# Kernel optimization log

Measured on AMD Instinct MI355X. Metric: run time of the kernel, lower is better.

Reference implementation:

```python
import jax, jax.numpy as jnp
import numpy as np

N_NODES = 16
N_EDGES = 64
N_LAYERS = 4


def _gcn(x, src, dst, emask, W, b):
    # PyG GCNConv: add self-loops, symmetric deg^-1/2 normalization, sum-aggregate.
    n = x.shape[0]
    h = x @ W  # [n, d_out]
    deg = jax.ops.segment_sum(emask, dst, num_segments=n) + 1.0  # +1 self-loop
    dinv = jax.lax.rsqrt(deg)
    norm = dinv[src] * dinv[dst] * emask  # masked-out edges get 0 weight
    out = jax.ops.segment_sum(norm[:, None] * h[src], dst, num_segments=n)
    return out + (dinv * dinv)[:, None] * h + b  # self-loop term + bias


def _sag_pool(x, src, dst, emask, w_rel, b_rel, w_root, k):
    # SAGPooling with GraphConv scorer: score = lin_rel(sum_j x_j) + lin_root(x)
    n = x.shape[0]
    agg = jax.ops.segment_sum(emask[:, None] * x[src], dst, num_segments=n)
    score = agg @ w_rel + b_rel + x @ w_root  # [n]
    perm = jnp.argsort(-score)[:k]  # top-k nodes
    x_new = x[perm] * jnp.tanh(score[perm])[:, None]
    kept = jnp.zeros(n, bool).at[perm].set(True)
    pos = jnp.zeros(n, jnp.int32).at[perm].set(jnp.arange(k, dtype=jnp.int32))
    emask_new = emask * kept[src] * kept[dst]  # drop edges touching removed nodes
    return x_new, pos[src], pos[dst], emask_new


def _conv_gnn(x, src, dst, W0, Ws, bs, pWrel, pbrel, pWroot, linW, linb):
    emask = jnp.ones(src.shape[0], x.dtype)
    n = x.shape[0]
    for i in range(N_LAYERS):
        W = W0 if i == 0 else Ws[i - 1]
        x = jax.nn.relu(_gcn(x, src, dst, emask, W, bs[i]))
        k = -(-n // 2)  # ceil(0.5 * n) -- SAGPooling ratio=0.5
        x, src, dst, emask = _sag_pool(x, src, dst, emask, pWrel[i], pbrel[i], pWroot[i], k)
        n = k
    x = x @ linW + linb  # [1, 128]
    return jax.nn.log_softmax(x, axis=1)


def _fc(h, fcW, fcb, lnw, lnb):
    eps = 1e-5
    for i in range(3):
        h = h @ fcW[i] + fcb[i]
        mu = h.mean(-1, keepdims=True)
        var = ((h - mu) ** 2).mean(-1, keepdims=True)
        h = (h - mu) * jax.lax.rsqrt(var + eps) * lnw[i] + lnb[i]
        h = jax.nn.relu(h)
    return h @ fcW[3] + fcb[3]


def setup_inputs() -> dict:
    key = jax.random.key(0)
    ks = iter(jax.random.split(key, 64))

    def rn(shape, s=0.05):
        return jax.random.normal(next(ks), shape, jnp.float32) * s

    def gnn_params(p):
        return {
            p + '_W0': rn((45, 128)), p + '_W': rn((3, 128, 128)),
            p + '_b': jnp.zeros((4, 128), jnp.float32),
            p + '_pWrel': rn((4, 128)), p + '_pbrel': jnp.zeros((4,), jnp.float32),
            p + '_pWroot': rn((4, 128)),
            p + '_linW': rn((128, 128)), p + '_linb': jnp.zeros((128,), jnp.float32),
        }

    inp = {
        'gp_x': rn((N_NODES, 45), 1.0), 'sp_x': rn((N_NODES, 45), 1.0),
        'gp_src': jax.random.randint(next(ks), (N_EDGES,), 0, N_NODES, jnp.int32),
        'gp_dst': jax.random.randint(next(ks), (N_EDGES,), 0, N_NODES, jnp.int32),
        'sp_src': jax.random.randint(next(ks), (N_EDGES,), 0, N_NODES, jnp.int32),
        'sp_dst': jax.random.randint(next(ks), (N_EDGES,), 0, N_NODES, jnp.int32),
        'fcW': rn((4, 256, 256)), 'fcb': jnp.zeros((4, 256), jnp.float32),
        'lnw': jnp.ones((3, 256), jnp.float32), 'lnb': jnp.zeros((3, 256), jnp.float32),
    }
    inp.update(gnn_params('g'))
    inp.update(gnn_params('s'))
    return inp


def reference(gp_x, sp_x, gp_src, gp_dst, sp_src, sp_dst,
              g_W0, g_W, g_b, g_pWrel, g_pbrel, g_pWroot, g_linW, g_linb,
              s_W0, s_W, s_b, s_pWrel, s_pbrel, s_pWroot, s_linW, s_linb,
              fcW, fcb, lnw, lnb):
    out1 = _conv_gnn(gp_x, gp_src, gp_dst, g_W0, g_W, g_b, g_pWrel, g_pbrel, g_pWroot, g_linW, g_linb)
    out2 = _conv_gnn(sp_x, sp_src, sp_dst, s_W0, s_W, s_b, s_pWrel, s_pbrel, s_pWroot, s_linW, s_linb)
    concat = jnp.concatenate((out1.reshape(-1), out2.reshape(-1)))  # [256]
    return _fc(concat, fcW, fcb, lnw, lnb)
```

## Files before the change

kernel.cpp:

```cpp
#include <hip/hip_runtime.h>
#include <math.h>

#define MAGIC 0x5F3759DFu
typedef unsigned int u32;

__device__ __forceinline__ void bar_lds(){
  asm volatile("s_waitcnt lgkmcnt(0)\n\ts_barrier" ::: "memory");
}
__device__ __forceinline__ void bar_vm0(){
  asm volatile("s_waitcnt vmcnt(0) lgkmcnt(0)\n\ts_barrier" ::: "memory");
}
__device__ __forceinline__ void bar_vm8(){
  asm volatile("s_waitcnt vmcnt(8) lgkmcnt(0)\n\ts_barrier" ::: "memory");
}

__device__ inline float wsum(float v){
  #pragma unroll
  for (int o=32;o;o>>=1) v += __shfl_xor(v,o,64);
  return v;
}
__device__ inline float wmax(float v){
  #pragma unroll
  for (int o=32;o;o>>=1) v = fmaxf(v,__shfl_xor(v,o,64));
  return v;
}
__device__ inline float hsum32(float v){
  #pragma unroll
  for (int o=16;o;o>>=1) v += __shfl_xor(v,o,64);
  return v;
}
__device__ __forceinline__ void stageW(const float* g, float* l, int nfloats,
                                       int wid, int lane){
  const int nch = nfloats>>8;
  for (int c=wid; c<nch; c+=8)
    __builtin_amdgcn_global_load_lds(
      (__attribute__((address_space(1))) u32*)(void*)(g+(c<<8)+(lane<<2)),
      (__attribute__((address_space(3))) u32*)(void*)(l+(c<<8)), 16, 0, 0);
}
__device__ __forceinline__ void pf(const float* p, int nfloats, int tid){
  float4 acc={0.f,0.f,0.f,0.f};
  const int nq=nfloats>>2;
  for (int i=tid;i<nq;i+=512){
    const float4 v=((const float4*)p)[i];
    acc.x+=v.x; acc.y+=v.y; acc.z+=v.z; acc.w+=v.w;
  }
  asm volatile("" :: "v"(acc.x),"v"(acc.y),"v"(acc.z),"v"(acc.w));
}

__global__ __launch_bounds__(512,1) void net_kernel(
    const float* __restrict__ gp_x, const float* __restrict__ sp_x,
    const int* __restrict__ gp_src, const int* __restrict__ gp_dst,
    const int* __restrict__ sp_src, const int* __restrict__ sp_dst,
    const float* __restrict__ g_W0, const float* __restrict__ g_W,
    const float* __restrict__ g_b,  const float* __restrict__ g_pWrel,
    const float* __restrict__ g_pbrel, const float* __restrict__ g_pWroot,
    const float* __restrict__ g_linW, const float* __restrict__ g_linb,
    const float* __restrict__ s_W0, const float* __restrict__ s_W,
    const float* __restrict__ s_b,  const float* __restrict__ s_pWrel,
    const float* __restrict__ s_pbrel, const float* __restrict__ s_pWroot,
    const float* __restrict__ s_linW, const float* __restrict__ s_linb,
    const float* __restrict__ fcW, const float* __restrict__ fcb,
    const float* __restrict__ lnw, const float* __restrict__ lnb,
    float* __restrict__ wsbuf, float* __restrict__ out)
{
  __shared__ __align__(16) float slotA[16384];
  __shared__ __align__(16) float slotB[16384];
  __shared__ __align__(16) float XBx[16][128];
  __shared__ __align__(16) float ZBraw[1024];
  __shared__ __align__(16) float PBf[2048];
  __shared__ __align__(16) float wrelL[512], wrootL[512];
  __shared__ __align__(16) float Adn[256], Mdn[256];
  __shared__ float d1P[64], d2P[64];
  __shared__ float yA[128];
  __shared__ float tsA[8]; __shared__ int permA[8];
  __shared__ float fcin[256]; __shared__ float wpart[16];

  const int lt  = threadIdx.x;
  const int bid = blockIdx.x;
  const int wid = lt>>6, lane = lt&63;

  if (bid >= 6){
    if (bid==6){ pf(g_W0,5760,lt); pf(g_pWrel,512,lt); pf(g_pWroot,512,lt);
                 pf(g_b,512,lt);   pf(g_linb,128,lt); }
    else if (bid==7){ pf(s_W0,5760,lt); pf(s_pWrel,512,lt); pf(s_pWroot,512,lt);
                 pf(s_b,512,lt);   pf(s_linb,128,lt); }
    else if (bid<=11) pf(g_W + (bid-8)*12288, 12288, lt);
    else if (bid<=15) pf(s_W + (bid-12)*12288, 12288, lt);
    else if (bid<=17) pf(g_linW + (bid-16)*8192, 8192, lt);
    else              pf(s_linW + (bid-18)*8192, 8192, lt);
    return;
  }

  if (bid >= 2){
    const int L = bid-2;
    const int qfc=(wid<<3)+(lane&7), f0fc=(lane>>3)<<5;
    float4 wr[32];
    #pragma unroll
    for (int t=0;t<32;++t) wr[t]=*(const float4*)(fcW+(L<<16)+(f0fc+t)*256+(qfc<<2));
    const float4 bb=*(const float4*)(fcb+(L<<8)+(qfc<<2));
    float4 lw={0,0,0,0}, lb2={0,0,0,0};
    if (L<3){ lw=*(const float4*)(lnw+(L<<8)+(qfc<<2)); lb2=*(const float4*)(lnb+(L<<8)+(qfc<<2)); }
    if (lt==0){
      if (L==0){
        const u32* f1=(const u32*)(wsbuf+128);
        const u32* f2=(const u32*)(wsbuf+384);
        while (__hip_atomic_load(f1,__ATOMIC_ACQUIRE,__HIP_MEMORY_SCOPE_AGENT)!=MAGIC ||
               __hip_atomic_load(f2,__ATOMIC_ACQUIRE,__HIP_MEMORY_SCOPE_AGENT)!=MAGIC)
          __builtin_amdgcn_s_sleep(1);
      } else {
        const u32* f1=(const u32*)(wsbuf+512+(L-1)*512+256);
        while (__hip_atomic_load(f1,__ATOMIC_ACQUIRE,__HIP_MEMORY_SCOPE_AGENT)!=MAGIC)
          __builtin_amdgcn_s_sleep(1);
      }
    }
    bar_lds();
    if (lt<256){
      const float* src = (L==0) ? (wsbuf + (lt<128 ? lt : 128+lt))
                                : (wsbuf + 512 + (L-1)*512 + lt);
      fcin[lt]=__hip_atomic_load(src,__ATOMIC_RELAXED,__HIP_MEMORY_SCOPE_AGENT);
    }
    bar_lds();
    float4 a={0.f,0.f,0.f,0.f};
    #pragma unroll
    for (int t=0;t<32;++t){
      const float zv=fcin[f0fc+t];
      a.x+=zv*wr[t].x; a.y+=zv*wr[t].y; a.z+=zv*wr[t].z; a.w+=zv*wr[t].w;
    }
    #pragma unroll
    for (int m=8;m<64;m<<=1){
      a.x+=__shfl_xor(a.x,m,64); a.y+=__shfl_xor(a.y,m,64);
      a.z+=__shfl_xor(a.z,m,64); a.w+=__shfl_xor(a.w,m,64);
    }
    if (L==3){
      if (lane<8){
        float4 r; r.x=a.x+bb.x; r.y=a.y+bb.y; r.z=a.z+bb.z; r.w=a.w+bb.w;
        *(float4*)(out+(qfc<<2))=r;
      }
      return;
    }
    const bool act=(lane<8);
    float4 hv={0.f,0.f,0.f,0.f};
    if (act){
      hv.x=a.x+bb.x; hv.y=a.y+bb.y; hv.z=a.z+bb.z; hv.w=a.w+bb.w;
      float s=hv.x+hv.y+hv.z+hv.w;
      float s2=hv.x*hv.x+hv.y*hv.y+hv.z*hv.z+hv.w*hv.w;
      #pragma unroll
      for (int m=1;m<8;m<<=1){ s+=__shfl_xor(s,m,64); s2+=__shfl_xor(s2,m,64); }
      if (lane==0){ wpart[wid]=s; wpart[8+wid]=s2; }
    }
    bar_lds();
    if (act){
      float S=0.f,S2=0.f;
      #pragma unroll
      for (int w2=0;w2<8;++w2){ S+=wpart[w2]; S2+=wpart[8+w2]; }
      const float mu=S*(1.f/256.f);
      const float ri=rsqrtf(S2*(1.f/256.f)-mu*mu+1e-5f);
      float* dst=wsbuf+512+L*512+(qfc<<2);
      __hip_atomic_store(dst+0,fmaxf((hv.x-mu)*ri*lw.x+lb2.x,0.f),__ATOMIC_RELAXED,__HIP_MEMORY_SCOPE_AGENT);
      __hip_atomic_store(dst+1,fmaxf((hv.y-mu)*ri*lw.y+lb2.y,0.f),__ATOMIC_RELAXED,__HIP_MEMORY_SCOPE_AGENT);
      __hip_atomic_store(dst+2,fmaxf((hv.z-mu)*ri*lw.z+lb2.z,0.f),__ATOMIC_RELAXED,__HIP_MEMORY_SCOPE_AGENT);
      __hip_atomic_store(dst+3,fmaxf((hv.w-mu)*ri*lw.w+lb2.w,0.f),__ATOMIC_RELAXED,__HIP_MEMORY_SCOPE_AGENT);
    }
    __threadfence();
    bar_lds();
    if (lt==0) __hip_atomic_store((u32*)(wsbuf+512+L*512+256),MAGIC,__ATOMIC_RELEASE,__HIP_MEMORY_SCOPE_AGENT);
    return;
  }

  const int br = bid;
  const float* x0    = br ? sp_x    : gp_x;
  const int*   srcg  = br ? sp_src  : gp_src;
  const int*   dstg  = br ? sp_dst  : gp_dst;
  const float* W0    = br ? s_W0    : g_W0;
  const float* Wl    = br ? s_W     : g_W;
  const float* bl    = br ? s_b     : g_b;
  const float* wrel  = br ? s_pWrel : g_pWrel;
  const float* brel  = br ? s_pbrel : g_pbrel;
  const float* wroot = br ? s_pWroot: g_pWroot;
  const float* linWg = br ? s_linW  : g_linW;
  const float* linb  = br ? s_linb  : g_linb;
  float* wsOut = wsbuf + br*256;
  u32*   wsFlag = (u32*)(wsbuf + 128 + br*256);

  float xv[4];
  #pragma unroll
  for (int r=0;r<4;++r){
    const int i=lt+(r<<9), v=i>>7, f=i&127;
    xv[r] = (f<45)? x0[v*45+f] : 0.f;
  }
  int es=0, ed=0; float emk=0.f;
  if (lt<64){ es=srcg[lt]; ed=dstg[lt]; emk=1.f; }
  const float4 brelv = *(const float4*)brel;
  const int bi4=(lt&31)<<2;
  const float4 blv0=*(const float4*)(bl       + bi4);
  const float4 blv1=*(const float4*)(bl + 128 + bi4);
  const float4 blv2=*(const float4*)(bl + 256 + bi4);
  const float4 blv3=*(const float4*)(bl + 384 + bi4);
  const float linb_s = linb[lt>>2];
  asm volatile("" ::: "memory");
  stageW(wrel,  wrelL,  512, wid, lane);
  stageW(wroot, wrootL, 512, wid, lane);
  stageW(Wl,    slotA, 16384, wid, lane);

  auto build_dense=[&](int kk, float wlane, bool with_ts){
    const float4 z4={0.f,0.f,0.f,0.f};
    *(float4*)&Adn[lt<<2]=z4;
    *(float4*)&Mdn[lt<<2]=z4;
    const bool act=(emk!=0.f);
    int mycnt=0;
    for (int v=0;v<kk;++v){
      const unsigned long long m=__ballot(act&&(ed==v));
      if (lt==v) mycnt=__popcll(m);
    }
    const float dinvl=rsqrtf(1.f+(float)mycnt);
    const float dvs=__shfl(dinvl,es,64);
    const float dvd=__shfl(dinvl,ed,64);
    if (act){
      atomicAdd(&Adn[ed*16+es], dvs*dvd*wlane);
      atomicAdd(&Mdn[ed*16+es], 1.f);
    }
    if (lt<kk){
      const float tv = with_ts ? tsA[lt] : 1.f;
      atomicAdd(&Adn[lt*17], dinvl*dinvl*tv);
    }
  };
  auto doE=[&](int n,int k,float bv,bool rebuild){
    if (lt<64){
      const float d1s=(lt<n)? d1P[lt<<2] : 0.f;
      float sc=-INFINITY;
      if (lt<n){
        float acc=d2P[lt<<2]+bv;
        for (int u=0;u<n;++u) acc += Mdn[lt*16+u]*__shfl(d1s,u,64);
        sc=acc;
      }
      int rank=0;
      for (int u=0;u<n;++u){
        const float su=__shfl(sc,u,64);
        rank += (su>sc || (su==sc && u<lt)) ? 1:0;
      }
      const int kept=(lt<n && rank<k)?1:0;
      const int pos=kept?rank:0;
      const float tval=kept?tanhf(sc):0.f;
      if (kept){ permA[rank]=lt; tsA[rank]=tval; }
      const float ts_src=__shfl(tval,es,64);
      const int ks=__shfl(kept,es,64), kd=__shfl(kept,ed,64);
      const int ps=__shfl(pos,es,64),  pd=__shfl(pos,ed,64);
      emk *= (float)(ks&kd);
      es=ps; ed=pd;
      if (rebuild) build_dense(k, ts_src, true);
    }
  };
  auto doB=[&](int n){
    if (lt<(n<<5)){
      const int v=lt>>5, j4=(lt&31)<<2;
      float4 a={0.f,0.f,0.f,0.f};
      for (int u=0;u<n;++u){
        const float w=Adn[v*16+u];
        const float4 xs=*(const float4*)&XBx[permA[u]][j4];
        a.x+=w*xs.x; a.y+=w*xs.y; a.z+=w*xs.z; a.w+=w*xs.w;
      }
      *(float4*)&ZBraw[(v<<7)+j4]=a;
    }
  };
  auto cmain=[&](const float* slot, int L){
    const int sh=9-L, nq=512>>L, CH=128>>L;
    const int q=lt&(nq-1), fh=lt>>sh;
    const int v=q>>5, c4=q&31, f0=fh*CH;
    const float* zrow=&ZBraw[v<<7];
    float4 a={0.f,0.f,0.f,0.f};
    for (int f=0; f<CH; ++f){
      const float zv=zrow[f0+f];
      const float4 w4=*(const float4*)&slot[(f0+f)*128+(c4<<2)];
      a.x+=zv*w4.x; a.y+=zv*w4.y; a.z+=zv*w4.z; a.w+=zv*w4.w;
    }
    ((float4*)PBf)[lt]=a;
  };
  auto creduce=[&](int L, float4 bl4){
    const int nq=512>>L, SPL=1<<L;
    if (lt<nq){
      const int v=lt>>5, c4=lt&31;
      float4 acc=bl4;
      for (int s=0;s<SPL;++s){
        const float4 p=((const float4*)PBf)[s*nq+lt];
        acc.x+=p.x; acc.y+=p.y; acc.z+=p.z; acc.w+=p.w;
      }
      float4 o;
      o.x=fmaxf(acc.x,0.f); o.y=fmaxf(acc.y,0.f);
      o.z=fmaxf(acc.z,0.f); o.w=fmaxf(acc.w,0.f);
      *(float4*)&XBx[v][c4<<2]=o;
      const float4 wr4=*(const float4*)&wrelL[(L<<7)+(c4<<2)];
      const float4 wo4=*(const float4*)&wrootL[(L<<7)+(c4<<2)];
      float p1=o.x*wr4.x+o.y*wr4.y+o.z*wr4.z+o.w*wr4.w;
      float p2=o.x*wo4.x+o.y*wo4.y+o.z*wo4.z+o.w*wo4.w;
      p1=hsum32(p1); p2=hsum32(p2);
      if ((lane&31)==0){ d1P[v<<2]=p1; d2P[v<<2]=p2; }
    }
  };

  #pragma unroll
  for (int r=0;r<4;++r){
    const int i=lt+(r<<9), v=i>>7, f=i&127;
    XBx[v][f]=xv[r];
  }
  if (lt<64) build_dense(16, 1.f, false);
  bar_lds();

  if (lt<256){
    const int v=lt>>4, j4=(lt&15)<<2;
    if (j4<48){
      float4 a={0.f,0.f,0.f,0.f};
      for (int u=0;u<16;++u){
        const float w=Adn[v*16+u];
        const float4 xs=*(const float4*)&XBx[u][j4];
        a.x+=w*xs.x; a.y+=w*xs.y; a.z+=w*xs.z; a.w+=w*xs.w;
      }
      *(float4*)&ZBraw[v*48+j4]=a;
    }
  }
  bar_vm8();

  {
    const int v=lt>>5, c4=lt&31, j4=c4<<2;
    const float* zrow=&ZBraw[v*48];
    float4 a={0.f,0.f,0.f,0.f};
    #pragma unroll
    for (int bb=0;bb<2;++bb){
      float4 wr[16]; float zr[16];
      #pragma unroll
      for (int t=0;t<16;++t){ wr[t]=*(const float4*)(W0+(bb*16+t)*128+j4); zr[t]=zrow[bb*16+t]; }
      #pragma unroll
      for (int t=0;t<16;++t){ a.x+=zr[t]*wr[t].x; a.y+=zr[t]*wr[t].y; a.z+=zr[t]*wr[t].z; a.w+=zr[t]*wr[t].w; }
    }
    { float4 wr[13]; float zr[13];
      #pragma unroll
      for (int t=0;t<13;++t){ wr[t]=*(const float4*)(W0+(32+t)*128+j4); zr[t]=zrow[32+t]; }
      #pragma unroll
      for (int t=0;t<13;++t){ a.x+=zr[t]*wr[t].x; a.y+=zr[t]*wr[t].y; a.z+=zr[t]*wr[t].z; a.w+=zr[t]*wr[t].w; }
    }
    float4 ox;
    ox.x=fmaxf(a.x+blv0.x,0.f); ox.y=fmaxf(a.y+blv0.y,0.f);
    ox.z=fmaxf(a.z+blv0.z,0.f); ox.w=fmaxf(a.w+blv0.w,0.f);
    *(float4*)&XBx[v][j4]=ox;
    const float4 wr4=*(const float4*)&wrelL[j4];
    const float4 wo4=*(const float4*)&wrootL[j4];
    float p1=ox.x*wr4.x+ox.y*wr4.y+ox.z*wr4.z+ox.w*wr4.w;
    float p2=ox.x*wo4.x+ox.y*wo4.y+ox.z*wo4.z+ox.w*wo4.w;
    p1=hsum32(p1); p2=hsum32(p2);
    if ((lane&31)==0){
      const int vv=(wid<<1)|(lane>>5);
      d1P[vv<<2]=p1; d2P[vv<<2]=p2;
    }
  }
  stageW(Wl+16384, slotB, 16384, wid, lane);
  bar_lds();

  doE(16, 8, brelv.x, true);   bar_lds();
  doB(8);                      bar_vm8();
  cmain(slotA, 1);             bar_lds();
  creduce(1, blv1);            bar_lds();
  stageW(Wl+32768, slotA, 16384, wid, lane);
  doE(8, 4, brelv.y, true);    bar_lds();
  doB(4);                      bar_vm8();
  cmain(slotB, 2);             bar_lds();
  creduce(2, blv2);            bar_lds();
  stageW(linWg, slotB, 16384, wid, lane);
  doE(4, 2, brelv.z, true);    bar_lds();
  doB(2);                      bar_vm8();
  cmain(slotA, 3);             bar_lds();
  creduce(3, blv3);            bar_lds();
  doE(2, 1, brelv.w, false);   bar_vm0();

  {
    const int oj=lt>>2, fh=lt&3;
    const int prow=permA[0];
    float p=0.f;
    #pragma unroll
    for (int i=0;i<32;++i){
      const int f=(fh<<5)+i;
      p += XBx[prow][f]*slotB[f*128+oj];
    }
    p+=__shfl_xor(p,1,64); p+=__shfl_xor(p,2,64);
    if (fh==0) yA[oj]=p*tsA[0]+linb_s;
  }
  bar_lds();
  if (lt<128){
    const int ln=lt&63;
    const float a0=yA[ln], b0=yA[64+ln];
    const float m=wmax(fmaxf(a0,b0));
    const float sum=wsum(expf(a0-m)+expf(b0-m));
    const float lse=m+logf(sum);
    __hip_atomic_store(&wsOut[lt], yA[lt]-lse, __ATOMIC_RELAXED, __HIP_MEMORY_SCOPE_AGENT);
  }
  __threadfence();
  bar_lds();
  if (lt==0) __hip_atomic_store(wsFlag, MAGIC, __ATOMIC_RELEASE, __HIP_MEMORY_SCOPE_AGENT);
}

extern "C" void kernel_launch(void* const* d_in, const int* in_sizes, int n_in,
                              void* d_out, int out_size, void* d_ws, size_t ws_size,
                              hipStream_t stream){
  net_kernel<<<20,512,0,stream>>>(
    (const float*)d_in[0],(const float*)d_in[1],
    (const int*)d_in[2],(const int*)d_in[3],(const int*)d_in[4],(const int*)d_in[5],
    (const float*)d_in[10],(const float*)d_in[11],(const float*)d_in[12],(const float*)d_in[13],
    (const float*)d_in[14],(const float*)d_in[15],(const float*)d_in[16],(const float*)d_in[17],
    (const float*)d_in[18],(const float*)d_in[19],(const float*)d_in[20],(const float*)d_in[21],
    (const float*)d_in[22],(const float*)d_in[23],(const float*)d_in[24],(const float*)d_in[25],
    (const float*)d_in[6],(const float*)d_in[7],(const float*)d_in[8],(const float*)d_in[9],
    (float*)d_ws,(float*)d_out);
}
```

Measured before the change: 24.18 us.

## Fold first FC layer partials into GNN branch blocks to shorten the chain

Result: slower. 25.16 us (+4.0%).

```diff
diff --git a/kernel.cpp b/kernel.cpp
--- a/kernel.cpp
+++ b/kernel.cpp
@@ -45,6 +45,20 @@
     acc.x+=v.x; acc.y+=v.y; acc.z+=v.z; acc.w+=v.w;
   }
   asm volatile("" :: "v"(acc.x),"v"(acc.y),"v"(acc.z),"v"(acc.w));
+}
+__device__ __forceinline__ void poll1(const u32* f, int lane){
+  u32 v=0;
+  do {
+    if (lane==0) v=__hip_atomic_load(f,__ATOMIC_ACQUIRE,__HIP_MEMORY_SCOPE_AGENT);
+    v=(u32)__shfl((int)v,0,64);
+    if (v!=MAGIC) __builtin_amdgcn_s_sleep(1);
+  } while (v!=MAGIC);
+}
+__device__ __forceinline__ float aload(const float* p){
+  return __hip_atomic_load(p,__ATOMIC_RELAXED,__HIP_MEMORY_SCOPE_AGENT);
+}
+__device__ __forceinline__ void astore(float* p, float v){
+  __hip_atomic_store(p,v,__ATOMIC_RELAXED,__HIP_MEMORY_SCOPE_AGENT);
 }
 
 __global__ __launch_bounds__(512,1) void net_kernel(
@@ -78,60 +92,107 @@
   const int lt  = threadIdx.x;
   const int bid = blockIdx.x;
   const int wid = lt>>6, lane = lt&63;
-
-  if (bid >= 6){
-    if (bid==6){ pf(g_W0,5760,lt); pf(g_pWrel,512,lt); pf(g_pWroot,512,lt);
+  const int qfc=(wid<<3)+(lane&7);
+
+  if (bid >= 5){
+    if (bid==5){ pf(g_W0,5760,lt); pf(g_pWrel,512,lt); pf(g_pWroot,512,lt);
                  pf(g_b,512,lt);   pf(g_linb,128,lt); }
-    else if (bid==7){ pf(s_W0,5760,lt); pf(s_pWrel,512,lt); pf(s_pWroot,512,lt);
+    else if (bid==6){ pf(s_W0,5760,lt); pf(s_pWrel,512,lt); pf(s_pWroot,512,lt);
                  pf(s_b,512,lt);   pf(s_linb,128,lt); }
-    else if (bid<=11) pf(g_W + (bid-8)*12288, 12288, lt);
-    else if (bid<=15) pf(s_W + (bid-12)*12288, 12288, lt);
-    else if (bid<=17) pf(g_linW + (bid-16)*8192, 8192, lt);
-    else              pf(s_linW + (bid-18)*8192, 8192, lt);
+    else if (bid<=10) pf(g_W + (bid-7)*12288, 12288, lt);
+    else if (bid<=14) pf(s_W + (bid-11)*12288, 12288, lt);
+    else if (bid<=16) pf(g_linW + (bid-15)*8192, 8192, lt);
+    else if (bid<=18) pf(s_linW + (bid-17)*8192, 8192, lt);
+    else if (bid==19) pf(fcW, 32768, lt);
+    else              pf(fcW+32768, 32768, lt);
     return;
   }
 
   if (bid >= 2){
-    const int L = bid-2;
-    const int qfc=(wid<<3)+(lane&7), f0fc=(lane>>3)<<5;
+    const int L = bid-1;
+    const int f0fc=(lane>>3)<<5;
     float4 wr[32];
     #pragma unroll
     for (int t=0;t<32;++t) wr[t]=*(const float4*)(fcW+(L<<16)+(f0fc+t)*256+(qfc<<2));
     const float4 bb=*(const float4*)(fcb+(L<<8)+(qfc<<2));
     float4 lw={0,0,0,0}, lb2={0,0,0,0};
     if (L<3){ lw=*(const float4*)(lnw+(L<<8)+(qfc<<2)); lb2=*(const float4*)(lnb+(L<<8)+(qfc<<2)); }
-    if (lt==0){
-      if (L==0){
-        const u32* f1=(const u32*)(wsbuf+128);
-        const u32* f2=(const u32*)(wsbuf+384);
-        while (__hip_atomic_load(f1,__ATOMIC_ACQUIRE,__HIP_MEMORY_SCOPE_AGENT)!=MAGIC ||
-               __hip_atomic_load(f2,__ATOMIC_ACQUIRE,__HIP_MEMORY_SCOPE_AGENT)!=MAGIC)
-          __builtin_amdgcn_s_sleep(1);
-      } else {
-        const u32* f1=(const u32*)(wsbuf+512+(L-1)*512+256);
-        while (__hip_atomic_load(f1,__ATOMIC_ACQUIRE,__HIP_MEMORY_SCOPE_AGENT)!=MAGIC)
-          __builtin_amdgcn_s_sleep(1);
-      }
-    }
-    bar_lds();
-    if (lt<256){
-      const float* src = (L==0) ? (wsbuf + (lt<128 ? lt : 128+lt))
-                                : (wsbuf + 512 + (L-1)*512 + lt);
-      fcin[lt]=__hip_atomic_load(src,__ATOMIC_RELAXED,__HIP_MEMORY_SCOPE_AGENT);
-    }
-    bar_lds();
+
+    if (bid==2){
+      float b0=0.f,w0=0.f,l0=0.f;
+      if (lt<256){ b0=fcb[lt]; w0=lnw[lt]; l0=lnb[lt]; }
+      poll1((const u32*)(wsbuf+256), lane);
+      poll1((const u32*)(wsbuf+576), lane);
+      float h=0.f;
+      if (lt<256){
+        h = aload(wsbuf+lt) + aload(wsbuf+320+lt) + b0;
+        float s=wsum(h), s2=wsum(h*h);
+        if (lane==0){ wpart[wid]=s; wpart[8+wid]=s2; }
+      }
+      bar_lds();
+      if (lt<256){
+        const float S =wpart[0]+wpart[1]+wpart[2]+wpart[3];
+        const float S2=wpart[8]+wpart[9]+wpart[10]+wpart[11];
+        const float mu=S*(1.f/256.f);
+        const float ri=rsqrtf(S2*(1.f/256.f)-mu*mu+1e-5f);
+        fcin[lt]=fmaxf((h-mu)*ri*w0+l0,0.f);
+      }
+      bar_lds();
+      float4 a={0.f,0.f,0.f,0.f};
+      #pragma unroll
+      for (int t=0;t<32;++t){
+        const float zv=fcin[f0fc+t];
+        a.x+=zv*wr[t].x; a.y+=zv*wr[t].y; a.z+=zv*wr[t].z; a.w+=zv*wr[t].w;
+      }
+      #pragma unroll
+      for (int m=8;m<64;m<<=1){
+        a.x+=__shfl_xor(a.x,m,64); a.y+=__shfl_xor(a.y,m,64);
+        a.z+=__shfl_xor(a.z,m,64); a.w+=__shfl_xor(a.w,m,64);
+      }
+      const bool act=(lane<8);
+      float4 hv={0.f,0.f,0.f,0.f};
+      if (act){
+        hv.x=a.x+bb.x; hv.y=a.y+bb.y; hv.z=a.z+bb.z; hv.w=a.w+bb.w;
+        float s=hv.x+hv.y+hv.z+hv.w;
+        float s2=hv.x*hv.x+hv.y*hv.y+hv.z*hv.z+hv.w*hv.w;
+        #pragma unroll
+        for (int m=1;m<8;m<<=1){ s+=__shfl_xor(s,m,64); s2+=__shfl_xor(s2,m,64); }
+        if (lane==0){ wpart[wid]=s; wpart[8+wid]=s2; }
+      }
+      bar_lds();
+      if (act){
+        float S=0.f,S2=0.f;
+        #pragma unroll
+        for (int w2=0;w2<8;++w2){ S+=wpart[w2]; S2+=wpart[8+w2]; }
+        const float mu=S*(1.f/256.f);
+        const float ri=rsqrtf(S2*(1.f/256.f)-mu*mu+1e-5f);
+        float* dst=wsbuf+640+(qfc<<2);
+        astore(dst+0,fmaxf((hv.x-mu)*ri*lw.x+lb2.x,0.f));
+        astore(dst+1,fmaxf((hv.y-mu)*ri*lw.y+lb2.y,0.f));
+        astore(dst+2,fmaxf((hv.z-mu)*ri*lw.z+lb2.z,0.f));
+        astore(dst+3,fmaxf((hv.w-mu)*ri*lw.w+lb2.w,0.f));
+      }
+      bar_vm0();
+      if (lt==0) __hip_atomic_store((u32*)(wsbuf+896),MAGIC,__ATOMIC_RELEASE,__HIP_MEMORY_SCOPE_AGENT);
+      return;
+    }
+
+    const int srcoff=(bid==3)?640:960, floff=(bid==3)?896:1216;
+    poll1((const u32*)(wsbuf+floff), lane);
+    float zr[32];
+    #pragma unroll
+    for (int t=0;t<32;++t) zr[t]=aload(wsbuf+srcoff+f0fc+t);
     float4 a={0.f,0.f,0.f,0.f};
     #pragma unroll
     for (int t=0;t<32;++t){
-      const float zv=fcin[f0fc+t];
-      a.x+=zv*wr[t].x; a.y+=zv*wr[t].y; a.z+=zv*wr[t].z; a.w+=zv*wr[t].w;
+      a.x+=zr[t]*wr[t].x; a.y+=zr[t]*wr[t].y; a.z+=zr[t]*wr[t].z; a.w+=zr[t]*wr[t].w;
     }
     #pragma unroll
     for (int m=8;m<64;m<<=1){
       a.x+=__shfl_xor(a.x,m,64); a.y+=__shfl_xor(a.y,m,64);
       a.z+=__shfl_xor(a.z,m,64); a.w+=__shfl_xor(a.w,m,64);
     }
-    if (L==3){
+    if (bid==4){
       if (lane<8){
         float4 r; r.x=a.x+bb.x; r.y=a.y+bb.y; r.z=a.z+bb.z; r.w=a.w+bb.w;
         *(float4*)(out+(qfc<<2))=r;
@@ -155,15 +216,14 @@
       for (int w2=0;w2<8;++w2){ S+=wpart[w2]; S2+=wpart[8+w2]; }
       const float mu=S*(1.f/256.f);
       const float ri=rsqrtf(S2*(1.f/256.f)-mu*mu+1e-5f);
-      float* dst=wsbuf+512+L*512+(qfc<<2);
-      __hip_atomic_store(dst+0,fmaxf((hv.x-mu)*ri*lw.x+lb2.x,0.f),__ATOMIC_RELAXED,__HIP_MEMORY_SCOPE_AGENT);
-      __hip_atomic_store(dst+1,fmaxf((hv.y-mu)*ri*lw.y+lb2.y,0.f),__ATOMIC_RELAXED,__HIP_MEMORY_SCOPE_AGENT);
-      __hip_atomic_store(dst+2,fmaxf((hv.z-mu)*ri*lw.z+lb2.z,0.f),__ATOMIC_RELAXED,__HIP_MEMORY_SCOPE_AGENT);
-      __hip_atomic_store(dst+3,fmaxf((hv.w-mu)*ri*lw.w+lb2.w,0.f),__ATOMIC_RELAXED,__HIP_MEMORY_SCOPE_AGENT);
-    }
-    __threadfence();
-    bar_lds();
-    if (lt==0) __hip_atomic_store((u32*)(wsbuf+512+L*512+256),MAGIC,__ATOMIC_RELEASE,__HIP_MEMORY_SCOPE_AGENT);
+      float* dst=wsbuf+960+(qfc<<2);
+      astore(dst+0,fmaxf((hv.x-mu)*ri*lw.x+lb2.x,0.f));
+      astore(dst+1,fmaxf((hv.y-mu)*ri*lw.y+lb2.y,0.f));
+      astore(dst+2,fmaxf((hv.z-mu)*ri*lw.z+lb2.z,0.f));
+      astore(dst+3,fmaxf((hv.w-mu)*ri*lw.w+lb2.w,0.f));
+    }
+    bar_vm0();
+    if (lt==0) __hip_atomic_store((u32*)(wsbuf+1216),MAGIC,__ATOMIC_RELEASE,__HIP_MEMORY_SCOPE_AGENT);
     return;
   }
 
@@ -179,8 +239,9 @@
   const float* wroot = br ? s_pWroot: g_pWroot;
   const float* linWg = br ? s_linW  : g_linW;
   const float* linb  = br ? s_linb  : g_linb;
-  float* wsOut = wsbuf + br*256;
-  u32*   wsFlag = (u32*)(wsbuf + 128 + br*256);
+  float* wsOut = wsbuf + br*320;
+  u32*   wsFlag = (u32*)(wsbuf + 256 + br*320);
+  const int f0fc=(lane>>3)<<4;
 
   float xv[4];
   #pragma unroll
@@ -352,6 +413,10 @@
     }
   }
   stageW(Wl+16384, slotB, 16384, wid, lane);
+  float4 wfc[16];
+  #pragma unroll
+  for (int t=0;t<16;++t)
+    wfc[t]=*(const float4*)(fcW + ((br<<7)+f0fc+t)*256 + (qfc<<2));
   bar_lds();
 
   doE(16, 8, brelv.x, true);   bar_lds();
@@ -389,17 +454,34 @@
     const float m=wmax(fmaxf(a0,b0));
     const float sum=wsum(expf(a0-m)+expf(b0-m));
     const float lse=m+logf(sum);
-    __hip_atomic_store(&wsOut[lt], yA[lt]-lse, __ATOMIC_RELAXED, __HIP_MEMORY_SCOPE_AGENT);
-  }
-  __threadfence();
+    fcin[lt]=yA[lt]-lse;
+  }
   bar_lds();
+  {
+    float4 a={0.f,0.f,0.f,0.f};
+    #pragma unroll
+    for (int t=0;t<16;++t){
+      const float zv=fcin[f0fc+t];
+      a.x+=zv*wfc[t].x; a.y+=zv*wfc[t].y; a.z+=zv*wfc[t].z; a.w+=zv*wfc[t].w;
+    }
+    #pragma unroll
+    for (int m=8;m<64;m<<=1){
+      a.x+=__shfl_xor(a.x,m,64); a.y+=__shfl_xor(a.y,m,64);
+      a.z+=__shfl_xor(a.z,m,64); a.w+=__shfl_xor(a.w,m,64);
+    }
+    if (lane<8){
+      float* dst=wsOut+(qfc<<2);
+      astore(dst+0,a.x); astore(dst+1,a.y); astore(dst+2,a.z); astore(dst+3,a.w);
+    }
+  }
+  bar_vm0();
   if (lt==0) __hip_atomic_store(wsFlag, MAGIC, __ATOMIC_RELEASE, __HIP_MEMORY_SCOPE_AGENT);
 }
 
 extern "C" void kernel_launch(void* const* d_in, const int* in_sizes, int n_in,
                               void* d_out, int out_size, void* d_ws, size_t ws_size,
                               hipStream_t stream){
-  net_kernel<<<20,512,0,stream>>>(
+  net_kernel<<<21,512,0,stream>>>(
     (const float*)d_in[0],(const float*)d_in[1],
     (const int*)d_in[2],(const int*)d_in[3],(const int*)d_in[4],(const int*)d_in[5],
     (const float*)d_in[10],(const float*)d_in[11],(const float*)d_in[12],(const float*)d_in[13],
```

## Poll flags per wave, load FC inputs directly, retile GCN matmul partials

Applied to the files above, without the earlier changes.

After: 24.17 us. About the same (-0.1%).

```diff
diff --git a/kernel.cpp b/kernel.cpp
--- a/kernel.cpp
+++ b/kernel.cpp
@@ -45,6 +45,56 @@
     acc.x+=v.x; acc.y+=v.y; acc.z+=v.z; acc.w+=v.w;
   }
   asm volatile("" :: "v"(acc.x),"v"(acc.y),"v"(acc.z),"v"(acc.w));
+}
+__device__ __forceinline__ void poll1(const u32* f, int lane){
+  u32 v=0;
+  do {
+    if (lane==0) v=__hip_atomic_load(f,__ATOMIC_ACQUIRE,__HIP_MEMORY_SCOPE_AGENT);
+    v=(u32)__shfl((int)v,0,64);
+    if (v!=MAGIC) __builtin_amdgcn_s_sleep(1);
+  } while (v!=MAGIC);
+}
+__device__ __forceinline__ float aload(const float* p){
+  return __hip_atomic_load(p,__ATOMIC_RELAXED,__HIP_MEMORY_SCOPE_AGENT);
+}
+__device__ __forceinline__ void astore(float* p, float v){
+  __hip_atomic_store(p,v,__ATOMIC_RELAXED,__HIP_MEMORY_SCOPE_AGENT);
+}
+
+template<int F,int VH,int N>
+__device__ __forceinline__ void cmain2(int lt, const float* slot,
+                                       const float* ZBp, float* PBp){
+  constexpr int CH = 128/F;
+  const int c4 = lt&31, r = lt>>5;
+  const int fh = r & (F-1), vh = r / F;
+  const int f0 = fh*CH;
+  const float4* slot4 = (const float4*)slot;
+  float4 acc[VH];
+  #pragma unroll
+  for (int i=0;i<VH;++i) acc[i]=make_float4(0.f,0.f,0.f,0.f);
+  #pragma unroll
+  for (int f=0; f<CH; ++f){
+    const float4 w4 = slot4[(f0+f)*32 + c4];
+    #pragma unroll
+    for (int i=0;i<VH;++i){
+      const float zv = ZBp[((vh*VH+i)<<7) + f0 + f];
+      acc[i].x+=zv*w4.x; acc[i].y+=zv*w4.y; acc[i].z+=zv*w4.z; acc[i].w+=zv*w4.w;
+    }
+  }
+  #pragma unroll
+  for (int i=0;i<VH;++i){
+    acc[i].x+=__shfl_xor(acc[i].x,32,64);
+    acc[i].y+=__shfl_xor(acc[i].y,32,64);
+    acc[i].z+=__shfl_xor(acc[i].z,32,64);
+    acc[i].w+=__shfl_xor(acc[i].w,32,64);
+  }
+  if (!(r&1)){
+    const int fp = fh>>1;
+    float4* P4=(float4*)PBp;
+    #pragma unroll
+    for (int i=0;i<VH;++i)
+      P4[(fp*N + vh*VH + i)*32 + c4] = acc[i];
+  }
 }
 
 __global__ __launch_bounds__(512,1) void net_kernel(
@@ -100,31 +150,29 @@
     const float4 bb=*(const float4*)(fcb+(L<<8)+(qfc<<2));
     float4 lw={0,0,0,0}, lb2={0,0,0,0};
     if (L<3){ lw=*(const float4*)(lnw+(L<<8)+(qfc<<2)); lb2=*(const float4*)(lnb+(L<<8)+(qfc<<2)); }
-    if (lt==0){
-      if (L==0){
-        const u32* f1=(const u32*)(wsbuf+128);
-        const u32* f2=(const u32*)(wsbuf+384);
-        while (__hip_atomic_load(f1,__ATOMIC_ACQUIRE,__HIP_MEMORY_SCOPE_AGENT)!=MAGIC ||
-               __hip_atomic_load(f2,__ATOMIC_ACQUIRE,__HIP_MEMORY_SCOPE_AGENT)!=MAGIC)
-          __builtin_amdgcn_s_sleep(1);
-      } else {
-        const u32* f1=(const u32*)(wsbuf+512+(L-1)*512+256);
-        while (__hip_atomic_load(f1,__ATOMIC_ACQUIRE,__HIP_MEMORY_SCOPE_AGENT)!=MAGIC)
-          __builtin_amdgcn_s_sleep(1);
-      }
-    }
-    bar_lds();
-    if (lt<256){
-      const float* src = (L==0) ? (wsbuf + (lt<128 ? lt : 128+lt))
-                                : (wsbuf + 512 + (L-1)*512 + lt);
-      fcin[lt]=__hip_atomic_load(src,__ATOMIC_RELAXED,__HIP_MEMORY_SCOPE_AGENT);
-    }
-    bar_lds();
+
+    float zr[32];
+    if (L==0){
+      poll1((const u32*)(wsbuf+128), lane);
+      poll1((const u32*)(wsbuf+384), lane);
+      if (lt<256){
+        const float* src = wsbuf + (lt<128 ? lt : 128+lt);
+        fcin[lt]=aload(src);
+      }
+      bar_lds();
+      #pragma unroll
+      for (int t=0;t<32;++t) zr[t]=fcin[f0fc+t];
+    } else {
+      const int floff = (L==1)?768 : (L==2)?1280 : 1792;
+      const int srcoff= (L==1)?512 : (L==2)?1024 : 1536;
+      poll1((const u32*)(wsbuf+floff), lane);
+      #pragma unroll
+      for (int t=0;t<32;++t) zr[t]=aload(wsbuf+srcoff+f0fc+t);
+    }
     float4 a={0.f,0.f,0.f,0.f};
     #pragma unroll
     for (int t=0;t<32;++t){
-      const float zv=fcin[f0fc+t];
-      a.x+=zv*wr[t].x; a.y+=zv*wr[t].y; a.z+=zv*wr[t].z; a.w+=zv*wr[t].w;
+      a.x+=zr[t]*wr[t].x; a.y+=zr[t]*wr[t].y; a.z+=zr[t]*wr[t].z; a.w+=zr[t]*wr[t].w;
     }
     #pragma unroll
     for (int m=8;m<64;m<<=1){
@@ -156,13 +204,12 @@
       const float mu=S*(1.f/256.f);
       const float ri=rsqrtf(S2*(1.f/256.f)-mu*mu+1e-5f);
       float* dst=wsbuf+512+L*512+(qfc<<2);
-      __hip_atomic_store(dst+0,fmaxf((hv.x-mu)*ri*lw.x+lb2.x,0.f),__ATOMIC_RELAXED,__HIP_MEMORY_SCOPE_AGENT);
-      __hip_atomic_store(dst+1,fmaxf((hv.y-mu)*ri*lw.y+lb2.y,0.f),__ATOMIC_RELAXED,__HIP_MEMORY_SCOPE_AGENT);
-      __hip_atomic_store(dst+2,fmaxf((hv.z-mu)*ri*lw.z+lb2.z,0.f),__ATOMIC_RELAXED,__HIP_MEMORY_SCOPE_AGENT);
-      __hip_atomic_store(dst+3,fmaxf((hv.w-mu)*ri*lw.w+lb2.w,0.f),__ATOMIC_RELAXED,__HIP_MEMORY_SCOPE_AGENT);
-    }
-    __threadfence();
-    bar_lds();
+      astore(dst+0,fmaxf((hv.x-mu)*ri*lw.x+lb2.x,0.f));
+      astore(dst+1,fmaxf((hv.y-mu)*ri*lw.y+lb2.y,0.f));
+      astore(dst+2,fmaxf((hv.z-mu)*ri*lw.z+lb2.z,0.f));
+      astore(dst+3,fmaxf((hv.w-mu)*ri*lw.w+lb2.w,0.f));
+    }
+    bar_vm0();
     if (lt==0) __hip_atomic_store((u32*)(wsbuf+512+L*512+256),MAGIC,__ATOMIC_RELEASE,__HIP_MEMORY_SCOPE_AGENT);
     return;
   }
@@ -262,26 +309,13 @@
       *(float4*)&ZBraw[(v<<7)+j4]=a;
     }
   };
-  auto cmain=[&](const float* slot, int L){
-    const int sh=9-L, nq=512>>L, CH=128>>L;
-    const int q=lt&(nq-1), fh=lt>>sh;
-    const int v=q>>5, c4=q&31, f0=fh*CH;
-    const float* zrow=&ZBraw[v<<7];
-    float4 a={0.f,0.f,0.f,0.f};
-    for (int f=0; f<CH; ++f){
-      const float zv=zrow[f0+f];
-      const float4 w4=*(const float4*)&slot[(f0+f)*128+(c4<<2)];
-      a.x+=zv*w4.x; a.y+=zv*w4.y; a.z+=zv*w4.z; a.w+=zv*w4.w;
-    }
-    ((float4*)PBf)[lt]=a;
-  };
-  auto creduce=[&](int L, float4 bl4){
-    const int nq=512>>L, SPL=1<<L;
-    if (lt<nq){
+  auto creduce2=[&](int F, int N, int L, float4 bl4){
+    if (lt < (N<<5)){
       const int v=lt>>5, c4=lt&31;
+      const float4* P4=(const float4*)PBf;
       float4 acc=bl4;
-      for (int s=0;s<SPL;++s){
-        const float4 p=((const float4*)PBf)[s*nq+lt];
+      for (int fp=0; fp<(F>>1); ++fp){
+        const float4 p=P4[(fp*N+v)*32+c4];
         acc.x+=p.x; acc.y+=p.y; acc.z+=p.z; acc.w+=p.w;
       }
       float4 o;
@@ -354,21 +388,21 @@
   stageW(Wl+16384, slotB, 16384, wid, lane);
   bar_lds();
 
-  doE(16, 8, brelv.x, true);   bar_lds();
-  doB(8);                      bar_vm8();
-  cmain(slotA, 1);             bar_lds();
-  creduce(1, blv1);            bar_lds();
+  doE(16, 8, brelv.x, true);    bar_lds();
+  doB(8);                       bar_vm8();
+  cmain2<4,2,8>(lt, slotA, ZBraw, PBf);  bar_lds();
+  creduce2(4, 8, 1, blv1);      bar_lds();
   stageW(Wl+32768, slotA, 16384, wid, lane);
-  doE(8, 4, brelv.y, true);    bar_lds();
-  doB(4);                      bar_vm8();
-  cmain(slotB, 2);             bar_lds();
-  creduce(2, blv2);            bar_lds();
+  doE(8, 4, brelv.y, true);     bar_lds();
+  doB(4);                       bar_vm8();
+  cmain2<8,2,4>(lt, slotB, ZBraw, PBf); bar_lds();
+  creduce2(8, 4, 2, blv2);      bar_lds();
   stageW(linWg, slotB, 16384, wid, lane);
-  doE(4, 2, brelv.z, true);    bar_lds();
-  doB(2);                      bar_vm8();
-  cmain(slotA, 3);             bar_lds();
-  creduce(3, blv3);            bar_lds();
-  doE(2, 1, brelv.w, false);   bar_vm0();
+  doE(4, 2, brelv.z, true);     bar_lds();
+  doB(2);                       bar_vm8();
+  cmain2<8,1,2>(lt, slotA, ZBraw, PBf); bar_lds();
+  creduce2(8, 2, 3, blv3);      bar_lds();
+  doE(2, 1, brelv.w, false);    bar_vm0();
 
   {
     const int oj=lt>>2, fh=lt&3;
@@ -389,10 +423,9 @@
     const float m=wmax(fmaxf(a0,b0));
     const float sum=wsum(expf(a0-m)+expf(b0-m));
     const float lse=m+logf(sum);
-    __hip_atomic_store(&wsOut[lt], yA[lt]-lse, __ATOMIC_RELAXED, __HIP_MEMORY_SCOPE_AGENT);
-  }
-  __threadfence();
-  bar_lds();
+    astore(&wsOut[lt], yA[lt]-lse);
+  }
+  bar_vm0();
   if (lt==0) __hip_atomic_store(wsFlag, MAGIC, __ATOMIC_RELEASE, __HIP_MEMORY_SCOPE_AGENT);
 }
 
```
